# Kernel tuning notes

Hardware: AMD Instinct MI355X
Metric: run time of the kernel (lower is better)

## Reference

```python
import jax, jax.numpy as jnp
import numpy as np

N_NODES = 100000
N_RAND_EDGES = 1200000
IN_DIM = 64
K = 10  # number of propagation hops


def setup_inputs() -> dict:
    key = jax.random.key(0)
    k1, k2, k3, k4 = jax.random.split(key, 4)
    feats = jax.random.normal(k1, (N_NODES, IN_DIM), dtype=jnp.float32)
    # xavier_uniform with sigmoid gain (=1.0) for s: bound = sqrt(6/(fan_in+fan_out))
    bound = float(np.sqrt(6.0 / (IN_DIM + 1)))
    s = jax.random.uniform(k2, (IN_DIM, 1), dtype=jnp.float32, minval=-bound, maxval=bound)
    src_r = jax.random.randint(k3, (N_RAND_EDGES,), 0, N_NODES)
    dst_r = jax.random.randint(k4, (N_RAND_EDGES,), 0, N_NODES)
    loops = jnp.arange(N_NODES)
    # append self-loops so every node has in_degree >= 1 (finite deg^-0.5)
    src = jnp.concatenate([src_r, loops]).astype(jnp.int64)
    dst = jnp.concatenate([dst_r, loops]).astype(jnp.int64)
    return {"feats": feats, "s": s, "src": src, "dst": dst}


def reference(feats, s, src, dst):
    n = feats.shape[0]
    ones = jnp.ones(src.shape[0], dtype=feats.dtype)
    degs = jax.ops.segment_sum(ones, dst, num_segments=n)  # in-degrees [N]
    norm = (degs ** -0.5)[:, None]  # [N,1]
    results = [feats]
    h = feats
    for _ in range(K):
        h = h * norm                                        # pre-scale
        h = jax.ops.segment_sum(h[src], dst, num_segments=n)  # copy_u + sum SpMM
        h = h * norm                                        # post-scale
        results.append(h)
    H = jnp.stack(results, axis=1)  # [N, K+1, D]
    S = jax.nn.sigmoid(jnp.einsum('nkd,do->nk', H, s))  # [N, K+1] gates
    return jnp.einsum('nk,nkd->nd', S, H)  # [N, D]
```

## Files before the change

### kernel.cpp

```cpp
#include <hip/hip_runtime.h>
#include <hip/hip_bf16.h>
#include <hip/hip_fp16.h>
#include <math.h>


#define DIM 64
#define BSH 9
#define BSZ 512
#define MAXNB 256
#define A2_CHUNK 4096

__global__ void zero_int_kernel(int* __restrict__ p, int n) {
    int i = blockIdx.x * blockDim.x + threadIdx.x;
    if (i < n) p[i] = 0;
}

__global__ void bin_count_kernel(const int* __restrict__ dst,
                                 int* __restrict__ binCount, int E) {
    __shared__ int lb[MAXNB];
    if (threadIdx.x < MAXNB) lb[threadIdx.x] = 0;
    __syncthreads();
    for (int e = blockIdx.x * blockDim.x + threadIdx.x; e < E;
         e += gridDim.x * blockDim.x) {
        atomicAdd(&lb[dst[e] >> BSH], 1);
    }
    __syncthreads();
    if (threadIdx.x < MAXNB && lb[threadIdx.x])
        atomicAdd(&binCount[threadIdx.x], lb[threadIdx.x]);
}

__global__ void binscan_kernel(const int* __restrict__ binCount,
                               int* __restrict__ binBase, int* __restrict__ tail,
                               int* __restrict__ rp, int NB, int N, int E) {
    __shared__ int lds[256];
    int t = threadIdx.x;
    int v = (t < NB) ? binCount[t] : 0;
    lds[t] = v;
    __syncthreads();
    for (int off = 1; off < 256; off <<= 1) {
        int x = (t >= off) ? lds[t - off] : 0;
        __syncthreads();
        lds[t] += x;
        __syncthreads();
    }
    int excl = lds[t] - v;
    if (t < NB) { binBase[t] = excl; tail[t] = excl; }
    if (t == 0) { binBase[NB] = E; rp[N] = E; }
}

__global__ void bin_scatter_kernel(const int* __restrict__ src,
                                   const int* __restrict__ dst,
                                   int* __restrict__ tail,
                                   int2* __restrict__ pairs, int E) {
    __shared__ int cnt[MAXNB];
    __shared__ int base[MAXNB];
    int t = threadIdx.x;
    int begE = blockIdx.x * A2_CHUNK;
    int endE = begE + A2_CHUNK; if (endE > E) endE = E;
    if (t < MAXNB) cnt[t] = 0;
    __syncthreads();
    for (int e = begE + t; e < endE; e += blockDim.x)
        atomicAdd(&cnt[dst[e] >> BSH], 1);
    __syncthreads();
    if (t < MAXNB) {
        int c = cnt[t];
        base[t] = c ? atomicAdd(&tail[t], c) : 0;
        cnt[t] = 0;
    }
    __syncthreads();
    for (int e = begE + t; e < endE; e += blockDim.x) {
        int d = dst[e];
        int b = d >> BSH;
        int pos = base[b] + atomicAdd(&cnt[b], 1);
        pairs[pos] = make_int2(src[e], d);
    }
}

__global__ void bucket_build_kernel(const int2* __restrict__ pairs,
                                    const int* __restrict__ binBase,
                                    int* __restrict__ col, int* __restrict__ rp,
                                    float* __restrict__ norm, int N) {
    __shared__ int degL[BSZ];
    __shared__ int off[BSZ];
    __shared__ int tmp[256];
    int b  = blockIdx.x;
    int lo = b << BSH;
    int cnt = N - lo; if (cnt > BSZ) cnt = BSZ;
    int t = threadIdx.x;
    degL[t] = 0; degL[t + 256] = 0;
    __syncthreads();
    int rbeg = binBase[b], rend = binBase[b + 1];
    for (int j = rbeg + t; j < rend; j += 256)
        atomicAdd(&degL[pairs[j].y - lo], 1);
    __syncthreads();
    int d0 = degL[2 * t], d1 = degL[2 * t + 1];
    int s2 = d0 + d1;
    tmp[t] = s2;
    __syncthreads();
    for (int o = 1; o < 256; o <<= 1) {
        int x = (t >= o) ? tmp[t - o] : 0;
        __syncthreads();
        tmp[t] += x;
        __syncthreads();
    }
    int e2 = tmp[t] - s2;
    off[2 * t]     = e2;
    off[2 * t + 1] = e2 + d0;
    __syncthreads();
    if (2 * t < cnt) {
        rp[lo + 2 * t] = rbeg + e2;
        norm[lo + 2 * t] = rsqrtf((float)d0);
    }
    if (2 * t + 1 < cnt) {
        rp[lo + 2 * t + 1] = rbeg + e2 + d0;
        norm[lo + 2 * t + 1] = rsqrtf((float)d1);
    }
    for (int j = rbeg + t; j < rend; j += 256) {
        int2 p = pairs[j];
        int slot = atomicAdd(&off[p.y - lo], 1);
        col[rbeg + slot] = p.x;
    }
}

__global__ void init_w0_kernel(const float* __restrict__ feats,
                               const float* __restrict__ norm,
                               __half* __restrict__ w, int N) {
    int n = blockIdx.x * (blockDim.x >> 6) + (threadIdx.x >> 6);
    int lane = threadIdx.x & 63;
    if (n >= N) return;
    size_t idx = ((size_t)n << 6) + lane;
    w[idx] = __float2half(feats[idx] * norm[n]);
}

__global__ void gather_hop_store_kernel(const __half* __restrict__ w,
                                        const int* __restrict__ rp,
                                        const int* __restrict__ col,
                                        const float* __restrict__ norm,
                                        __half* __restrict__ wnext, int N) {
    int wid  = (blockIdx.x * blockDim.x + threadIdx.x) >> 6;
    int lane = threadIdx.x & 63;
    int g    = lane >> 3;
    int sub  = lane & 7;
    int gbase = lane & 56;
    int n    = (wid << 3) + g;
    bool valid = (n < N);
    int nc = valid ? n : (N - 1);

    int beg = rp[nc];
    int end = rp[nc + 1];
    int deg = valid ? (end - beg) : 0;
    float nm = norm[nc];

    int maxdeg = deg;
    maxdeg = max(maxdeg, __shfl_xor(maxdeg, 8, 64));
    maxdeg = max(maxdeg, __shfl_xor(maxdeg, 16, 64));
    maxdeg = max(maxdeg, __shfl_xor(maxdeg, 32, 64));

    float acc[8];
    #pragma unroll
    for (int i = 0; i < 8; ++i) acc[i] = 0.0f;

    const __half* wsub = w + (sub << 3);

    for (int base = 0; base < maxdeg; base += 8) {
        int i0 = beg + base + sub;
        int c0 = (i0 < end) ? col[i0] : 0;
        #pragma unroll
        for (int jj = 0; jj < 8; jj += 2) {
            if (base + jj >= maxdeg) break;
            int ccA = __shfl(c0, gbase + jj, 64);
            int ccB = __shfl(c0, gbase + jj + 1, 64);
            float4 rA = *(const float4*)(wsub + ((size_t)ccA << 6));
            float4 rB = *(const float4*)(wsub + ((size_t)ccB << 6));
            if (base + jj < deg) {
                const __half2* h2 = (const __half2*)&rA;
                float2 f0 = __half22float2(h2[0]);
                float2 f1 = __half22float2(h2[1]);
                float2 f2 = __half22float2(h2[2]);
                float2 f3 = __half22float2(h2[3]);
                acc[0] += f0.x; acc[1] += f0.y;
                acc[2] += f1.x; acc[3] += f1.y;
                acc[4] += f2.x; acc[5] += f2.y;
                acc[6] += f3.x; acc[7] += f3.y;
            }
            if (base + jj + 1 < deg) {
                const __half2* h2 = (const __half2*)&rB;
                float2 f0 = __half22float2(h2[0]);
                float2 f1 = __half22float2(h2[1]);
                float2 f2 = __half22float2(h2[2]);
                float2 f3 = __half22float2(h2[3]);
                acc[0] += f0.x; acc[1] += f0.y;
                acc[2] += f1.x; acc[3] += f1.y;
                acc[4] += f2.x; acc[5] += f2.y;
                acc[6] += f3.x; acc[7] += f3.y;
            }
        }
    }

    if (valid) {
        float n2 = nm * nm;
        __half2 hv[4];
        hv[0] = __floats2half2_rn(acc[0] * n2, acc[1] * n2);
        hv[1] = __floats2half2_rn(acc[2] * n2, acc[3] * n2);
        hv[2] = __floats2half2_rn(acc[4] * n2, acc[5] * n2);
        hv[3] = __floats2half2_rn(acc[6] * n2, acc[7] * n2);
        *(float4*)(wnext + ((size_t)n << 6) + (sub << 3)) = *(const float4*)hv;
    }
}

__global__ void readout_kernel(const __half* __restrict__ wbase,
                               const float* __restrict__ norm,
                               const float* __restrict__ s,
                               float* __restrict__ out,
                               int N, int nk, size_t kstride) {
    int wid  = (blockIdx.x * blockDim.x + threadIdx.x) >> 6;
    int lane = threadIdx.x & 63;
    int g    = lane >> 3;
    int sub  = lane & 7;
    int n    = (wid << 3) + g;
    bool valid = (n < N);
    int nc = valid ? n : (N - 1);

    float4 sa = *(const float4*)(s + (sub << 3));
    float4 sb = *(const float4*)(s + (sub << 3) + 4);

    float inm = 1.0f / norm[nc];
    size_t rowoff = ((size_t)nc << 6) + (sub << 3);

    float acc[8];
    #pragma unroll
    for (int i = 0; i < 8; ++i) acc[i] = 0.0f;

    for (int k = 0; k < nk; ++k) {
        float4 raw = *(const float4*)(wbase + rowoff + (size_t)k * kstride);
        const __half2* h2 = (const __half2*)&raw;
        float2 f0 = __half22float2(h2[0]);
        float2 f1 = __half22float2(h2[1]);
        float2 f2 = __half22float2(h2[2]);
        float2 f3 = __half22float2(h2[3]);
        float p = f0.x * sa.x + f0.y * sa.y + f1.x * sa.z + f1.y * sa.w
                + f2.x * sb.x + f2.y * sb.y + f3.x * sb.z + f3.y * sb.w;
        p += __shfl_xor(p, 1, 64);
        p += __shfl_xor(p, 2, 64);
        p += __shfl_xor(p, 4, 64);
        float gate = 1.0f / (1.0f + expf(-p * inm));
        float g2 = gate * inm;
        acc[0] += g2 * f0.x; acc[1] += g2 * f0.y;
        acc[2] += g2 * f1.x; acc[3] += g2 * f1.y;
        acc[4] += g2 * f2.x; acc[5] += g2 * f2.y;
        acc[6] += g2 * f3.x; acc[7] += g2 * f3.y;
    }

    if (valid) {
        float4 o0 = make_float4(acc[0], acc[1], acc[2], acc[3]);
        float4 o1 = make_float4(acc[4], acc[5], acc[6], acc[7]);
        float4* o = (float4*)(out + rowoff);
        o[0] = o0; o[1] = o1;
    }
}

__global__ void init_kernel(const float* __restrict__ feats,
                            const float* __restrict__ norm,
                            const float* __restrict__ s,
                            float* __restrict__ out,
                            __half* __restrict__ w, int N) {
    int n = blockIdx.x * (blockDim.x >> 6) + (threadIdx.x >> 6);
    int lane = threadIdx.x & 63;
    if (n >= N) return;
    size_t idx = ((size_t)n << 6) + lane;
    float v = feats[idx];
    float p = v * s[lane];
    #pragma unroll
    for (int off = 32; off; off >>= 1) p += __shfl_xor(p, off, 64);
    float gate = 1.0f / (1.0f + expf(-p));
    out[idx] = gate * v;
    w[idx] = __float2half(v * norm[n]);
}

__global__ void gather_hop_kernel(const __half* __restrict__ w,
                                  const int* __restrict__ rp,
                                  const int* __restrict__ col,
                                  const float* __restrict__ norm,
                                  const float* __restrict__ s,
                                  float* __restrict__ out,
                                  __half* __restrict__ wnext,
                                  int N, int write_next) {
    int n = blockIdx.x * (blockDim.x >> 6) + (threadIdx.x >> 6);
    if (n >= N) return;
    int lane = threadIdx.x & 63;
    int e_sub = lane >> 3;
    int c     = lane & 7;

    int beg = rp[n];
    int end = rp[n + 1];

    float acc[8];
    #pragma unroll
    for (int i = 0; i < 8; ++i) acc[i] = 0.0f;

    for (int j = beg + e_sub; j < end; j += 8) {
        int cc = col[j];
        float4 raw = *(const float4*)(w + ((size_t)cc << 6) + (c << 3));
        const __half2* h2 = (const __half2*)&raw;
        float2 f0 = __half22float2(h2[0]);
        float2 f1 = __half22float2(h2[1]);
        float2 f2 = __half22float2(h2[2]);
        float2 f3 = __half22float2(h2[3]);
        acc[0] += f0.x; acc[1] += f0.y;
        acc[2] += f1.x; acc[3] += f1.y;
        acc[4] += f2.x; acc[5] += f2.y;
        acc[6] += f3.x; acc[7] += f3.y;
    }

    #pragma unroll
    for (int off = 8; off < 64; off <<= 1) {
        #pragma unroll
        for (int i = 0; i < 8; ++i) acc[i] += __shfl_xor(acc[i], off, 64);
    }

    float nm = norm[n];
    float v[8];
    #pragma unroll
    for (int i = 0; i < 8; ++i) v[i] = acc[i] * nm;

    float4 sa = *(const float4*)(s + (c << 3));
    float4 sb = *(const float4*)(s + (c << 3) + 4);
    float p = v[0] * sa.x + v[1] * sa.y + v[2] * sa.z + v[3] * sa.w
            + v[4] * sb.x + v[5] * sb.y + v[6] * sb.z + v[7] * sb.w;
    #pragma unroll
    for (int off = 1; off < 8; off <<= 1) p += __shfl_xor(p, off, 64);
    float gate = 1.0f / (1.0f + expf(-p));

    size_t base = ((size_t)n << 6) + (c << 3);
    if (e_sub == 0) {
        float4* o = (float4*)(out + base);
        float4 o0 = o[0], o1 = o[1];
        o0.x += gate * v[0]; o0.y += gate * v[1];
        o0.z += gate * v[2]; o0.w += gate * v[3];
        o1.x += gate * v[4]; o1.y += gate * v[5];
        o1.z += gate * v[6]; o1.w += gate * v[7];
        o[0] = o0; o[1] = o1;
    } else if (e_sub == 1 && write_next) {
        __half2 hv[4];
        hv[0] = __floats2half2_rn(v[0] * nm, v[1] * nm);
        hv[1] = __floats2half2_rn(v[2] * nm, v[3] * nm);
        hv[2] = __floats2half2_rn(v[4] * nm, v[5] * nm);
        hv[3] = __floats2half2_rn(v[6] * nm, v[7] * nm);
        *(float4*)(wnext + base) = *(const float4*)hv;
    }
}

extern "C" void kernel_launch(void* const* d_in, const int* in_sizes, int n_in,
                              void* d_out, int out_size, void* d_ws, size_t ws_size,
                              hipStream_t stream) {
    const float* feats = (const float*)d_in[0];
    const float* s     = (const float*)d_in[1];
    const int*   src   = (const int*)d_in[2];
    const int*   dst   = (const int*)d_in[3];
    float* out = (float*)d_out;

    const int N = in_sizes[0] / DIM;
    const int E = in_sizes[2];
    const int K = 10;
    const int NB = (N + BSZ - 1) >> BSH;

    const int BLK = 256;
    const int wavesPerBlk = BLK / 64;
    int nodeBlocks  = (N + wavesPerBlk - 1) / wavesPerBlk;
    int nodeBlocks8 = (N + wavesPerBlk * 8 - 1) / (wavesPerBlk * 8);
    int a2Blocks = (E + A2_CHUNK - 1) / A2_CHUNK;

    size_t stateElems = (size_t)N * DIM;
    size_t intCount = (size_t)(N + 1) + E + 256 + 257 + 256;
    size_t need_full = (size_t)N * 4 + (size_t)(K + 1) * stateElems * 2
                     + intCount * 4 + (size_t)E * 8 + 64;
    int full = (ws_size >= need_full) ? 1 : 0;
    int nbuf = full ? (K + 1) : 2;

    float*  norm    = (float*)d_ws;
    __half* wbase   = (__half*)(norm + N);
    int*    rp      = (int*)(wbase + (size_t)nbuf * stateElems);
    int*    col     = rp + (N + 1);
    int*    binCount= col + E;
    int*    binBase = binCount + 256;
    int*    tail    = binBase + 257;
    size_t  poff    = (size_t)((char*)(tail + 256) - (char*)d_ws);
    poff = (poff + 7) & ~(size_t)7;
    int2*   pairs   = (int2*)((char*)d_ws + poff);

    zero_int_kernel<<<1, 256, 0, stream>>>(binCount, 256);
    bin_count_kernel<<<512, BLK, 0, stream>>>(dst, binCount, E);
    binscan_kernel<<<1, 256, 0, stream>>>(binCount, binBase, tail, rp, NB, N, E);
    bin_scatter_kernel<<<a2Blocks, BLK, 0, stream>>>(src, dst, tail, pairs, E);
    bucket_build_kernel<<<NB, 256, 0, stream>>>(pairs, binBase, col, rp, norm, N);

    if (full) {
        init_w0_kernel<<<nodeBlocks, BLK, 0, stream>>>(feats, norm, wbase, N);
        for (int k = 0; k < K; ++k) {
            const __half* cur = wbase + (size_t)k * stateElems;
            __half* nxt = wbase + (size_t)(k + 1) * stateElems;
            gather_hop_store_kernel<<<nodeBlocks8, BLK, 0, stream>>>(cur, rp, col,
                                                                     norm, nxt, N);
        }
        readout_kernel<<<nodeBlocks8, BLK, 0, stream>>>(wbase, norm, s, out,
                                                        N, K + 1, stateElems);
    } else {
        __half* wA = wbase;
        __half* wB = wbase + stateElems;
        init_kernel<<<nodeBlocks, BLK, 0, stream>>>(feats, norm, s, out, wA, N);
        __half* cur = wA;
        __half* nxt = wB;
        for (int k = 0; k < K; ++k) {
            int write_next = (k < K - 1) ? 1 : 0;
            gather_hop_kernel<<<nodeBlocks, BLK, 0, stream>>>(cur, rp, col, norm, s,
                                                              out, nxt, N, write_next);
            __half* t = cur; cur = nxt; nxt = t;
        }
    }
}
```

Measured before the change: 442.3 us.

## Split hidden state into four 16-column quarter planes for cache-friendly gathers

The fp16 hop state moves from row-major [N,64] to four planes of 16 columns each, and the gather kernel is launched so that interleaved blocks each process a single quarter. Each plane is about 3.2 MB instead of 12.8 MB, so the randomly gathered neighbour rows are more likely to stay in L2. The cost is that every hop now reads the col indices four times, once per quarter, and issues narrower 8-byte loads. Col loads and the output stores also switch to nontemporal hints so they are less likely to evict the state from cache.

```diff
diff --git a/kernel.cpp b/kernel.cpp
--- a/kernel.cpp
+++ b/kernel.cpp
@@ -128,21 +128,24 @@
     int n = blockIdx.x * (blockDim.x >> 6) + (threadIdx.x >> 6);
     int lane = threadIdx.x & 63;
     if (n >= N) return;
-    size_t idx = ((size_t)n << 6) + lane;
-    w[idx] = __float2half(feats[idx] * norm[n]);
-}
-
-__global__ void gather_hop_store_kernel(const __half* __restrict__ w,
-                                        const int* __restrict__ rp,
-                                        const int* __restrict__ col,
-                                        const float* __restrict__ norm,
-                                        __half* __restrict__ wnext, int N) {
-    int wid  = (blockIdx.x * blockDim.x + threadIdx.x) >> 6;
+    float v = feats[((size_t)n << 6) + lane] * norm[n];
+    int q = lane >> 4, o = lane & 15;
+    w[((size_t)q * N + n) << 4 | o] = __float2half(v);
+}
+
+__global__ void gather_hop_q_kernel(const __half* __restrict__ w,
+                                    const int* __restrict__ rp,
+                                    const int* __restrict__ col,
+                                    const float* __restrict__ norm,
+                                    __half* __restrict__ wnext, int N) {
+    int b = blockIdx.x;
+    int q = (b & 7) >> 1;
+    int chunk = ((b >> 3) << 1) | (b & 1);
     int lane = threadIdx.x & 63;
-    int g    = lane >> 3;
-    int sub  = lane & 7;
-    int gbase = lane & 56;
-    int n    = (wid << 3) + g;
+    int g    = lane >> 2;
+    int sub  = lane & 3;
+    int gbase = lane & 60;
+    int n = (chunk << 6) + ((threadIdx.x >> 6) << 4) + g;
     bool valid = (n < N);
     int nc = valid ? n : (N - 1);
 
@@ -152,59 +155,41 @@
     float nm = norm[nc];
 
     int maxdeg = deg;
+    maxdeg = max(maxdeg, __shfl_xor(maxdeg, 4, 64));
     maxdeg = max(maxdeg, __shfl_xor(maxdeg, 8, 64));
     maxdeg = max(maxdeg, __shfl_xor(maxdeg, 16, 64));
     maxdeg = max(maxdeg, __shfl_xor(maxdeg, 32, 64));
 
-    float acc[8];
-    #pragma unroll
-    for (int i = 0; i < 8; ++i) acc[i] = 0.0f;
-
-    const __half* wsub = w + (sub << 3);
-
-    for (int base = 0; base < maxdeg; base += 8) {
+    float acc[4];
+    acc[0] = acc[1] = acc[2] = acc[3] = 0.0f;
+
+    const __half* wq = w + (((size_t)q * N) << 4) + (sub << 2);
+
+    for (int base = 0; base < maxdeg; base += 4) {
         int i0 = beg + base + sub;
-        int c0 = (i0 < end) ? col[i0] : 0;
+        int c0 = (i0 < end) ? __builtin_nontemporal_load(col + i0) : 0;
         #pragma unroll
-        for (int jj = 0; jj < 8; jj += 2) {
+        for (int jj = 0; jj < 4; ++jj) {
             if (base + jj >= maxdeg) break;
-            int ccA = __shfl(c0, gbase + jj, 64);
-            int ccB = __shfl(c0, gbase + jj + 1, 64);
-            float4 rA = *(const float4*)(wsub + ((size_t)ccA << 6));
-            float4 rB = *(const float4*)(wsub + ((size_t)ccB << 6));
+            int cc = __shfl(c0, gbase + jj, 64);
+            float2 r = *(const float2*)(wq + ((size_t)cc << 4));
             if (base + jj < deg) {
-                const __half2* h2 = (const __half2*)&rA;
+                const __half2* h2 = (const __half2*)&r;
                 float2 f0 = __half22float2(h2[0]);
                 float2 f1 = __half22float2(h2[1]);
-                float2 f2 = __half22float2(h2[2]);
-                float2 f3 = __half22float2(h2[3]);
                 acc[0] += f0.x; acc[1] += f0.y;
                 acc[2] += f1.x; acc[3] += f1.y;
-                acc[4] += f2.x; acc[5] += f2.y;
-                acc[6] += f3.x; acc[7] += f3.y;
-            }
-            if (base + jj + 1 < deg) {
-                const __half2* h2 = (const __half2*)&rB;
-                float2 f0 = __half22float2(h2[0]);
-                float2 f1 = __half22float2(h2[1]);
-                float2 f2 = __half22float2(h2[2]);
-                float2 f3 = __half22float2(h2[3]);
-                acc[0] += f0.x; acc[1] += f0.y;
-                acc[2] += f1.x; acc[3] += f1.y;
-                acc[4] += f2.x; acc[5] += f2.y;
-                acc[6] += f3.x; acc[7] += f3.y;
             }
         }
     }
 
     if (valid) {
         float n2 = nm * nm;
-        __half2 hv[4];
+        __half2 hv[2];
         hv[0] = __floats2half2_rn(acc[0] * n2, acc[1] * n2);
         hv[1] = __floats2half2_rn(acc[2] * n2, acc[3] * n2);
-        hv[2] = __floats2half2_rn(acc[4] * n2, acc[5] * n2);
-        hv[3] = __floats2half2_rn(acc[6] * n2, acc[7] * n2);
-        *(float4*)(wnext + ((size_t)n << 6) + (sub << 3)) = *(const float4*)hv;
+        double* dstp = (double*)(wnext + ((((size_t)q * N + n) << 4) + (sub << 2)));
+        __builtin_nontemporal_store(*(const double*)hv, dstp);
     }
 }
 
@@ -225,14 +210,14 @@
     float4 sb = *(const float4*)(s + (sub << 3) + 4);
 
     float inm = 1.0f / norm[nc];
-    size_t rowoff = ((size_t)nc << 6) + (sub << 3);
+    size_t qoff = ((((size_t)(sub >> 1) * N + nc) << 4) + ((sub & 1) << 3));
 
     float acc[8];
     #pragma unroll
     for (int i = 0; i < 8; ++i) acc[i] = 0.0f;
 
     for (int k = 0; k < nk; ++k) {
-        float4 raw = *(const float4*)(wbase + rowoff + (size_t)k * kstride);
+        float4 raw = *(const float4*)(wbase + qoff + (size_t)k * kstride);
         const __half2* h2 = (const __half2*)&raw;
         float2 f0 = __half22float2(h2[0]);
         float2 f1 = __half22float2(h2[1]);
@@ -254,7 +239,7 @@
     if (valid) {
         float4 o0 = make_float4(acc[0], acc[1], acc[2], acc[3]);
         float4 o1 = make_float4(acc[4], acc[5], acc[6], acc[7]);
-        float4* o = (float4*)(out + rowoff);
+        float4* o = (float4*)(out + ((size_t)nc << 6) + (sub << 3));
         o[0] = o0; o[1] = o1;
     }
 }
@@ -370,6 +355,9 @@
     int nodeBlocks8 = (N + wavesPerBlk * 8 - 1) / (wavesPerBlk * 8);
     int a2Blocks = (E + A2_CHUNK - 1) / A2_CHUNK;
 
+    int chunks = (N + 63) >> 6;
+    int hopBlocks = ((chunks + 1) >> 1) << 3;
+
     size_t stateElems = (size_t)N * DIM;
     size_t intCount = (size_t)(N + 1) + E + 256 + 257 + 256;
     size_t need_full = (size_t)N * 4 + (size_t)(K + 1) * stateElems * 2
@@ -399,8 +387,8 @@
         for (int k = 0; k < K; ++k) {
             const __half* cur = wbase + (size_t)k * stateElems;
             __half* nxt = wbase + (size_t)(k + 1) * stateElems;
-            gather_hop_store_kernel<<<nodeBlocks8, BLK, 0, stream>>>(cur, rp, col,
-                                                                     norm, nxt, N);
+            gather_hop_q_kernel<<<hopBlocks, BLK, 0, stream>>>(cur, rp, col,
+                                                               norm, nxt, N);
         }
         readout_kernel<<<nodeBlocks8, BLK, 0, stream>>>(wbase, norm, s, out,
                                                         N, K + 1, stateElems);
```

New measurement: 736.8 us. +66.6%, slower.

## Sort nodes by in-degree so each wave gathers similar-degree rows

Applied to the files above, without the earlier changes.

Adds a degree histogram, a descending-degree scan and a scatter that build a permutation of nodes grouped by in-degree. The gather kernel then reads its nodes through this permutation, so the 8 nodes sharing a wave have similar degrees and less divergent loop work is wasted on the per-wave max degree. The inner loop also drops the paired two-row prefetch and issues one load per edge, guarded by the degree check. This costs four extra small kernels and an extra indirection, gives up the locality of consecutive node ids for the output writes, and reuses the pairs buffer for the permutation.

```diff
diff --git a/kernel.cpp b/kernel.cpp
--- a/kernel.cpp
+++ b/kernel.cpp
@@ -9,6 +9,8 @@
 #define BSZ 512
 #define MAXNB 256
 #define A2_CHUNK 4096
+#define DBINS 64
+#define DCHUNK 2048
 
 __global__ void zero_int_kernel(int* __restrict__ p, int n) {
     int i = blockIdx.x * blockDim.x + threadIdx.x;
@@ -122,6 +124,69 @@
     }
 }
 
+__global__ void deg_hist_kernel(const int* __restrict__ rp,
+                                int* __restrict__ degCnt, int N) {
+    __shared__ int lb[DBINS];
+    if (threadIdx.x < DBINS) lb[threadIdx.x] = 0;
+    __syncthreads();
+    for (int n = blockIdx.x * blockDim.x + threadIdx.x; n < N;
+         n += gridDim.x * blockDim.x) {
+        int d = rp[n + 1] - rp[n];
+        int b = (d < DBINS) ? d : (DBINS - 1);
+        atomicAdd(&lb[b], 1);
+    }
+    __syncthreads();
+    if (threadIdx.x < DBINS && lb[threadIdx.x])
+        atomicAdd(&degCnt[threadIdx.x], lb[threadIdx.x]);
+}
+
+__global__ void deg_scan_kernel(const int* __restrict__ degCnt,
+                                int* __restrict__ degCur) {
+    __shared__ int lds[DBINS];
+    int t = threadIdx.x;
+    int rb = DBINS - 1 - t;
+    int v = degCnt[rb];
+    lds[t] = v;
+    __syncthreads();
+    for (int off = 1; off < DBINS; off <<= 1) {
+        int x = (t >= off) ? lds[t - off] : 0;
+        __syncthreads();
+        lds[t] += x;
+        __syncthreads();
+    }
+    degCur[rb] = lds[t] - v;
+}
+
+__global__ void deg_scatter_kernel(const int* __restrict__ rp,
+                                   int* __restrict__ degCur,
+                                   int* __restrict__ perm, int N) {
+    __shared__ int cnt[DBINS];
+    __shared__ int base[DBINS];
+    int t = threadIdx.x;
+    int beg = blockIdx.x * DCHUNK;
+    int endn = beg + DCHUNK; if (endn > N) endn = N;
+    if (t < DBINS) cnt[t] = 0;
+    __syncthreads();
+    for (int n = beg + t; n < endn; n += blockDim.x) {
+        int d = rp[n + 1] - rp[n];
+        int b = (d < DBINS) ? d : (DBINS - 1);
+        atomicAdd(&cnt[b], 1);
+    }
+    __syncthreads();
+    if (t < DBINS) {
+        int c = cnt[t];
+        base[t] = c ? atomicAdd(&degCur[t], c) : 0;
+        cnt[t] = 0;
+    }
+    __syncthreads();
+    for (int n = beg + t; n < endn; n += blockDim.x) {
+        int d = rp[n + 1] - rp[n];
+        int b = (d < DBINS) ? d : (DBINS - 1);
+        int pos = base[b] + atomicAdd(&cnt[b], 1);
+        perm[pos] = n;
+    }
+}
+
 __global__ void init_w0_kernel(const float* __restrict__ feats,
                                const float* __restrict__ norm,
                                __half* __restrict__ w, int N) {
@@ -132,24 +197,25 @@
     w[idx] = __float2half(feats[idx] * norm[n]);
 }
 
-__global__ void gather_hop_store_kernel(const __half* __restrict__ w,
-                                        const int* __restrict__ rp,
-                                        const int* __restrict__ col,
-                                        const float* __restrict__ norm,
-                                        __half* __restrict__ wnext, int N) {
+__global__ void gather_hop_perm_kernel(const __half* __restrict__ w,
+                                       const int* __restrict__ rp,
+                                       const int* __restrict__ col,
+                                       const float* __restrict__ norm,
+                                       const int* __restrict__ perm,
+                                       __half* __restrict__ wnext, int N) {
     int wid  = (blockIdx.x * blockDim.x + threadIdx.x) >> 6;
     int lane = threadIdx.x & 63;
     int g    = lane >> 3;
     int sub  = lane & 7;
     int gbase = lane & 56;
-    int n    = (wid << 3) + g;
-    bool valid = (n < N);
-    int nc = valid ? n : (N - 1);
-
-    int beg = rp[nc];
-    int end = rp[nc + 1];
+    int dense = (wid << 3) + g;
+    bool valid = (dense < N);
+    int n = perm[valid ? dense : (N - 1)];
+
+    int beg = rp[n];
+    int end = rp[n + 1];
     int deg = valid ? (end - beg) : 0;
-    float nm = norm[nc];
+    float nm = norm[n];
 
     int maxdeg = deg;
     maxdeg = max(maxdeg, __shfl_xor(maxdeg, 8, 64));
@@ -166,25 +232,12 @@
         int i0 = beg + base + sub;
         int c0 = (i0 < end) ? col[i0] : 0;
         #pragma unroll
-        for (int jj = 0; jj < 8; jj += 2) {
+        for (int jj = 0; jj < 8; ++jj) {
             if (base + jj >= maxdeg) break;
-            int ccA = __shfl(c0, gbase + jj, 64);
-            int ccB = __shfl(c0, gbase + jj + 1, 64);
-            float4 rA = *(const float4*)(wsub + ((size_t)ccA << 6));
-            float4 rB = *(const float4*)(wsub + ((size_t)ccB << 6));
+            int cc = __shfl(c0, gbase + jj, 64);
             if (base + jj < deg) {
-                const __half2* h2 = (const __half2*)&rA;
-                float2 f0 = __half22float2(h2[0]);
-                float2 f1 = __half22float2(h2[1]);
-                float2 f2 = __half22float2(h2[2]);
-                float2 f3 = __half22float2(h2[3]);
-                acc[0] += f0.x; acc[1] += f0.y;
-                acc[2] += f1.x; acc[3] += f1.y;
-                acc[4] += f2.x; acc[5] += f2.y;
-                acc[6] += f3.x; acc[7] += f3.y;
-            }
-            if (base + jj + 1 < deg) {
-                const __half2* h2 = (const __half2*)&rB;
+                float4 raw = *(const float4*)(wsub + ((size_t)cc << 6));
+                const __half2* h2 = (const __half2*)&raw;
                 float2 f0 = __half22float2(h2[0]);
                 float2 f1 = __half22float2(h2[1]);
                 float2 f2 = __half22float2(h2[2]);
@@ -368,7 +421,8 @@
     const int wavesPerBlk = BLK / 64;
     int nodeBlocks  = (N + wavesPerBlk - 1) / wavesPerBlk;
     int nodeBlocks8 = (N + wavesPerBlk * 8 - 1) / (wavesPerBlk * 8);
-    int a2Blocks = (E + A2_CHUNK - 1) / A2_CHUNK;
+    int a2Blocks  = (E + A2_CHUNK - 1) / A2_CHUNK;
+    int dScBlocks = (N + DCHUNK - 1) / DCHUNK;
 
     size_t stateElems = (size_t)N * DIM;
     size_t intCount = (size_t)(N + 1) + E + 256 + 257 + 256;
@@ -387,6 +441,9 @@
     size_t  poff    = (size_t)((char*)(tail + 256) - (char*)d_ws);
     poff = (poff + 7) & ~(size_t)7;
     int2*   pairs   = (int2*)((char*)d_ws + poff);
+    int*    perm    = (int*)pairs;
+    int*    degCnt  = perm + N;
+    int*    degCur  = degCnt + DBINS;
 
     zero_int_kernel<<<1, 256, 0, stream>>>(binCount, 256);
     bin_count_kernel<<<512, BLK, 0, stream>>>(dst, binCount, E);
@@ -395,12 +452,18 @@
     bucket_build_kernel<<<NB, 256, 0, stream>>>(pairs, binBase, col, rp, norm, N);
 
     if (full) {
+        zero_int_kernel<<<1, 128, 0, stream>>>(degCnt, 2 * DBINS);
+        deg_hist_kernel<<<128, BLK, 0, stream>>>(rp, degCnt, N);
+        deg_scan_kernel<<<1, DBINS, 0, stream>>>(degCnt, degCur);
+        deg_scatter_kernel<<<dScBlocks, BLK, 0, stream>>>(rp, degCur, perm, N);
+
         init_w0_kernel<<<nodeBlocks, BLK, 0, stream>>>(feats, norm, wbase, N);
         for (int k = 0; k < K; ++k) {
             const __half* cur = wbase + (size_t)k * stateElems;
             __half* nxt = wbase + (size_t)(k + 1) * stateElems;
-            gather_hop_store_kernel<<<nodeBlocks8, BLK, 0, stream>>>(cur, rp, col,
-                                                                     norm, nxt, N);
+            gather_hop_perm_kernel<<<nodeBlocks8, BLK, 0, stream>>>(cur, rp, col,
+                                                                    norm, perm,
+                                                                    nxt, N);
         }
         readout_kernel<<<nodeBlocks8, BLK, 0, stream>>>(wbase, norm, s, out,
                                                         N, K + 1, stateElems);
```

After: 451.1 us. No clear change (+2.0%).
